# Optimization experiments

Measured on AMD Instinct MI355X. Metric: run time of the kernel, lower is better.

Reference implementation:

```python
import jax, jax.numpy as jnp
import numpy as np


def setup_inputs() -> dict:
    key = jax.random.key(0)
    ks = jax.random.split(key, 8)
    B = 32768
    return {
        "x": jax.random.normal(ks[0], (B, 784), dtype=jnp.float32),
        "conv_w": jax.random.normal(ks[1], (3, 3), dtype=jnp.float32),
        "fc1_w": jax.random.normal(ks[2], (512, 676), dtype=jnp.float32) * 0.04,
        "fc1_b": jax.random.normal(ks[3], (512,), dtype=jnp.float32),
        "fc2_w": jax.random.normal(ks[4], (512, 512), dtype=jnp.float32) * 0.04,
        "fc2_b": jax.random.normal(ks[5], (512,), dtype=jnp.float32),
        "out_w": jax.random.normal(ks[6], (10, 512), dtype=jnp.float32) * 0.04,
        "out_b": jax.random.normal(ks[7], (10,), dtype=jnp.float32),
    }


def reference(x, conv_w, fc1_w, fc1_b, fc2_w, fc2_b, out_w, out_b):
    B = x.shape[0]
    img = x.reshape(B, 1, 28, 28)  # NCHW, single channel
    # Valid 3x3 cross-correlation (same math as the nested tensordot loop).
    kern = conv_w.reshape(1, 1, 3, 3)  # OIHW
    conv = jax.lax.conv_general_dilated(
        img, kern, window_strides=(1, 1), padding="VALID",
        dimension_numbers=("NCHW", "OIHW", "NCHW"))  # [B,1,26,26]
    h = conv.reshape(B, 26 * 26)
    h = jax.nn.relu(h @ fc1_w.T + fc1_b)
    h = jax.nn.relu(h @ fc2_w.T + fc2_b)
    return h @ out_w.T + out_b  # [B,10] logits
```

## Files before the change

kernel.cpp:

```cpp
#include <hip/hip_runtime.h>

typedef unsigned short ushort_t;
typedef __attribute__((ext_vector_type(8))) short bf16x8;
typedef __attribute__((ext_vector_type(4))) float f32x4;
typedef __attribute__((ext_vector_type(16))) float f32x16;

__device__ __forceinline__ unsigned short f2bf(float f) {
    union { float f; unsigned u; } v; v.f = f;
    unsigned r = v.u + 0x7FFFu + ((v.u >> 16) & 1u);
    return (unsigned short)(r >> 16);
}

__global__ __launch_bounds__(256) void prep_w(const float* __restrict__ fc1_w,
                                              const float* __restrict__ cw,
                                              const float* __restrict__ fc2_w,
                                              const float* __restrict__ out_w,
                                              ushort_t* __restrict__ W1,
                                              ushort_t* __restrict__ W2,
                                              ushort_t* __restrict__ W3) {
    const int idx = blockIdx.x * 256 + threadIdx.x;
    if (idx < 512 * 832) {
        int n = idx / 832, p = idx % 832;
        float acc = 0.f;
        if (p < 784) {
            int pr = p / 28, pc = p % 28;
#pragma unroll
            for (int dr = 0; dr < 3; ++dr) {
                int r = pr - dr;
                if (r < 0 || r >= 26) continue;
#pragma unroll
                for (int dc = 0; dc < 3; ++dc) {
                    int col = pc - dc;
                    if (col < 0 || col >= 26) continue;
                    acc += cw[dr * 3 + dc] * fc1_w[n * 676 + r * 26 + col];
                }
            }
        }
        W1[idx] = f2bf(acc);
    }
    if (idx < 512 * 512) W2[idx] = f2bf(fc2_w[idx]);
    if (idx < 16 * 512)  W3[idx] = (idx < 10 * 512) ? f2bf(out_w[idx]) : (ushort_t)0;
}

__global__ __launch_bounds__(512, 2) void mega2(const float* __restrict__ x,
                                                const ushort_t* __restrict__ W1,
                                                const ushort_t* __restrict__ W2,
                                                const ushort_t* __restrict__ W3,
                                                const float* __restrict__ b1,
                                                const float* __restrict__ b2,
                                                const float* __restrict__ ob,
                                                float* __restrict__ out) {
    extern __shared__ ushort_t smem[];
    ushort_t* xs = smem;
    ushort_t* hs = smem + 8192;

    const int tid = threadIdx.x;
    const int wave = tid >> 6, lane = tid & 63;
    const int r32 = lane & 31, khalf = lane >> 5;
    const int xrow = tid >> 3, xoct = tid & 7;
    const int m0 = blockIdx.x * 128;

    f32x16 acc[2][2][2];
#pragma unroll
    for (int a = 0; a < 2; ++a)
#pragma unroll
        for (int i = 0; i < 2; ++i)
#pragma unroll
            for (int j = 0; j < 2; ++j)
#pragma unroll
                for (int e = 0; e < 16; ++e) acc[a][i][j][e] = 0.f;

    f32x4 xv0[2], xv1[2];
    auto load_x = [&](int ks) {
        const int gc = ks * 64 + xoct * 8;
#pragma unroll
        for (int mh = 0; mh < 2; ++mh) {
            if (gc < 784) {
                const f32x4* p = (const f32x4*)&x[(size_t)(m0 + mh * 64 + xrow) * 784 + gc];
                xv0[mh] = __builtin_nontemporal_load(p);
                xv1[mh] = __builtin_nontemporal_load(p + 1);
            } else {
                xv0[mh] = (f32x4){0.f, 0.f, 0.f, 0.f};
                xv1[mh] = (f32x4){0.f, 0.f, 0.f, 0.f};
            }
        }
    };
    load_x(0);

    for (int ks = 0; ks < 13; ++ks) {
#pragma unroll
        for (int mh = 0; mh < 2; ++mh) {
            bf16x8 xv;
            xv[0] = (short)f2bf(xv0[mh].x); xv[1] = (short)f2bf(xv0[mh].y);
            xv[2] = (short)f2bf(xv0[mh].z); xv[3] = (short)f2bf(xv0[mh].w);
            xv[4] = (short)f2bf(xv1[mh].x); xv[5] = (short)f2bf(xv1[mh].y);
            xv[6] = (short)f2bf(xv1[mh].z); xv[7] = (short)f2bf(xv1[mh].w);
            *(bf16x8*)&xs[mh * 4096 + xrow * 64 + ((xoct ^ (xrow & 7)) * 8)] = xv;
        }
        __syncthreads();
        if (ks < 12) load_x(ks + 1);
        const int k0 = ks * 64;
#pragma unroll
        for (int ksub = 0; ksub < 4; ++ksub) {
            const int q = 2 * ksub + khalf;
            bf16x8 bw[2], af[2][2];
#pragma unroll
            for (int j = 0; j < 2; ++j)
                bw[j] = *(const bf16x8*)&W1[(size_t)(wave * 64 + j * 32 + r32) * 832 + k0 + q * 8];
#pragma unroll
            for (int mh = 0; mh < 2; ++mh)
#pragma unroll
                for (int i = 0; i < 2; ++i) {
                    const int mr = i * 32 + r32;
                    af[mh][i] = *(const bf16x8*)&xs[mh * 4096 + mr * 64 + ((q ^ (mr & 7)) * 8)];
                }
#pragma unroll
            for (int mh = 0; mh < 2; ++mh)
#pragma unroll
                for (int i = 0; i < 2; ++i)
#pragma unroll
                    for (int j = 0; j < 2; ++j)
                        acc[mh][i][j] = __builtin_amdgcn_mfma_f32_32x32x16_bf16(af[mh][i], bw[j], acc[mh][i][j], 0, 0, 0);
        }
        __syncthreads();
    }

#pragma unroll
    for (int j = 0; j < 2; ++j) {
        const int n = wave * 64 + j * 32 + r32;
        const float bb = b1[n];
        const int nseg = n >> 3, nrem = n & 7;
#pragma unroll
        for (int mh = 0; mh < 2; ++mh)
#pragma unroll
            for (int i = 0; i < 2; ++i)
#pragma unroll
                for (int reg = 0; reg < 16; ++reg) {
                    const int m = mh * 64 + i * 32 + 4 * khalf + (reg & 3) + 8 * (reg >> 2);
                    hs[m * 512 + ((nseg ^ (m & 7)) * 8) + nrem] = f2bf(fmaxf(acc[mh][i][j][reg] + bb, 0.f));
                }
    }
#pragma unroll
    for (int a = 0; a < 2; ++a)
#pragma unroll
        for (int i = 0; i < 2; ++i)
#pragma unroll
            for (int j = 0; j < 2; ++j)
#pragma unroll
                for (int e = 0; e < 16; ++e) acc[a][i][j][e] = 0.f;
    __syncthreads();

    for (int ks = 0; ks < 8; ++ks) {
        const int k0 = ks * 64;
#pragma unroll
        for (int ksub = 0; ksub < 4; ++ksub) {
            const int q = 2 * ksub + khalf;
            const int hq = ks * 8 + q;
            bf16x8 bw[2], af[2][2];
#pragma unroll
            for (int j = 0; j < 2; ++j)
                bw[j] = *(const bf16x8*)&W2[(size_t)(wave * 64 + j * 32 + r32) * 512 + k0 + q * 8];
#pragma unroll
            for (int mh = 0; mh < 2; ++mh)
#pragma unroll
                for (int i = 0; i < 2; ++i) {
                    const int m = mh * 64 + i * 32 + r32;
                    af[mh][i] = *(const bf16x8*)&hs[m * 512 + ((hq ^ (m & 7)) * 8)];
                }
#pragma unroll
            for (int mh = 0; mh < 2; ++mh)
#pragma unroll
                for (int i = 0; i < 2; ++i)
#pragma unroll
                    for (int j = 0; j < 2; ++j)
                        acc[mh][i][j] = __builtin_amdgcn_mfma_f32_32x32x16_bf16(af[mh][i], bw[j], acc[mh][i][j], 0, 0, 0);
        }
    }
    __syncthreads();

#pragma unroll
    for (int j = 0; j < 2; ++j) {
        const int n = wave * 64 + j * 32 + r32;
        const float bb = b2[n];
        const int nseg = n >> 3, nrem = n & 7;
#pragma unroll
        for (int mh = 0; mh < 2; ++mh)
#pragma unroll
            for (int i = 0; i < 2; ++i)
#pragma unroll
                for (int reg = 0; reg < 16; ++reg) {
                    const int m = mh * 64 + i * 32 + 4 * khalf + (reg & 3) + 8 * (reg >> 2);
                    hs[m * 512 + ((nseg ^ (m & 7)) * 8) + nrem] = f2bf(fmaxf(acc[mh][i][j][reg] + bb, 0.f));
                }
    }
    __syncthreads();

    {
        const int quad = lane >> 4, l16 = lane & 15;
        const int row = wave * 16 + l16;
        f32x4 hacc = {0.f, 0.f, 0.f, 0.f};
#pragma unroll
        for (int ks = 0; ks < 16; ++ks) {
            const int seg = 4 * ks + quad;
            const bf16x8 a = *(const bf16x8*)&hs[row * 512 + ((seg ^ (row & 7)) * 8)];
            const bf16x8 b = *(const bf16x8*)&W3[l16 * 512 + ks * 32 + quad * 8];
            hacc = __builtin_amdgcn_mfma_f32_16x16x32_bf16(a, b, hacc, 0, 0, 0);
        }
        if (l16 < 10) {
            const float bb = ob[l16];
#pragma unroll
            for (int r = 0; r < 4; ++r)
                out[(size_t)(m0 + wave * 16 + quad * 4 + r) * 10 + l16] = hacc[r] + bb;
        }
    }
}

extern "C" void kernel_launch(void* const* d_in, const int* in_sizes, int n_in,
                              void* d_out, int out_size, void* d_ws, size_t ws_size,
                              hipStream_t stream) {
    const float* x      = (const float*)d_in[0];
    const float* conv_w = (const float*)d_in[1];
    const float* fc1_w  = (const float*)d_in[2];
    const float* fc1_b  = (const float*)d_in[3];
    const float* fc2_w  = (const float*)d_in[4];
    const float* fc2_b  = (const float*)d_in[5];
    const float* out_w  = (const float*)d_in[6];
    const float* out_b  = (const float*)d_in[7];
    float* out = (float*)d_out;

    ushort_t* W1 = (ushort_t*)d_ws;
    ushort_t* W2 = W1 + 512 * 832;
    ushort_t* W3 = W2 + 512 * 512;

    prep_w<<<dim3(1664), 256, 0, stream>>>(fc1_w, conv_w, fc2_w, out_w, W1, W2, W3);

    mega2<<<dim3(256), 512, 147456, stream>>>(x, W1, W2, W3, fc1_b, fc2_b, out_b, out);
}
```

Before: 235.7 us.

## Pre-pack weights into MFMA fragment order and double-buffer x tiles

The weight prep kernel writes W1 and W2 in a per-wave fragment layout, so each lane's B-operand load is one contiguous 16-byte read and each wave reads a contiguous 1KB block. The x staging in shared memory is double-buffered, so the next tile is converted and stored while the current one is consumed, leaving one barrier per k-step instead of two. This costs extra shared memory, and the second x buffer reuses the region later used for the hidden activations.

```diff
diff --git a/kernel.cpp b/kernel.cpp
--- a/kernel.cpp
+++ b/kernel.cpp
@@ -36,13 +36,22 @@
                 }
             }
         }
-        W1[idx] = f2bf(acc);
-    }
-    if (idx < 512 * 512) W2[idx] = f2bf(fc2_w[idx]);
+        const int ngrp = n >> 5, r = n & 31;
+        const int kfrag = p >> 4, c = p & 15;
+        const int lane = (c >> 3) * 32 + r;
+        W1[((size_t)ngrp * 52 + kfrag) * 512 + lane * 8 + (c & 7)] = f2bf(acc);
+    }
+    if (idx < 512 * 512) {
+        int n = idx >> 9, p = idx & 511;
+        const int ngrp = n >> 5, r = n & 31;
+        const int kfrag = p >> 4, c = p & 15;
+        const int lane = (c >> 3) * 32 + r;
+        W2[((size_t)ngrp * 32 + kfrag) * 512 + lane * 8 + (c & 7)] = f2bf(fc2_w[idx]);
+    }
     if (idx < 16 * 512)  W3[idx] = (idx < 10 * 512) ? f2bf(out_w[idx]) : (ushort_t)0;
 }
 
-__global__ __launch_bounds__(512, 2) void mega2(const float* __restrict__ x,
+__global__ __launch_bounds__(512, 2) void mega3(const float* __restrict__ x,
                                                 const ushort_t* __restrict__ W1,
                                                 const ushort_t* __restrict__ W2,
                                                 const ushort_t* __restrict__ W3,
@@ -85,9 +94,7 @@
             }
         }
     };
-    load_x(0);
-
-    for (int ks = 0; ks < 13; ++ks) {
+    auto store_x = [&](int buf) {
 #pragma unroll
         for (int mh = 0; mh < 2; ++mh) {
             bf16x8 xv;
@@ -95,24 +102,31 @@
             xv[2] = (short)f2bf(xv0[mh].z); xv[3] = (short)f2bf(xv0[mh].w);
             xv[4] = (short)f2bf(xv1[mh].x); xv[5] = (short)f2bf(xv1[mh].y);
             xv[6] = (short)f2bf(xv1[mh].z); xv[7] = (short)f2bf(xv1[mh].w);
-            *(bf16x8*)&xs[mh * 4096 + xrow * 64 + ((xoct ^ (xrow & 7)) * 8)] = xv;
-        }
-        __syncthreads();
+            *(bf16x8*)&xs[buf * 8192 + mh * 4096 + xrow * 64 + ((xoct ^ (xrow & 7)) * 8)] = xv;
+        }
+    };
+
+    load_x(0);
+    store_x(0);
+    __syncthreads();
+
+    for (int ks = 0; ks < 13; ++ks) {
         if (ks < 12) load_x(ks + 1);
-        const int k0 = ks * 64;
+        const int buf = ks & 1;
 #pragma unroll
         for (int ksub = 0; ksub < 4; ++ksub) {
+            const int kfrag = ks * 4 + ksub;
+            bf16x8 bw[2], af[2][2];
+#pragma unroll
+            for (int j = 0; j < 2; ++j)
+                bw[j] = *(const bf16x8*)&W1[((size_t)(wave * 2 + j) * 52 + kfrag) * 512 + lane * 8];
             const int q = 2 * ksub + khalf;
-            bf16x8 bw[2], af[2][2];
-#pragma unroll
-            for (int j = 0; j < 2; ++j)
-                bw[j] = *(const bf16x8*)&W1[(size_t)(wave * 64 + j * 32 + r32) * 832 + k0 + q * 8];
 #pragma unroll
             for (int mh = 0; mh < 2; ++mh)
 #pragma unroll
                 for (int i = 0; i < 2; ++i) {
                     const int mr = i * 32 + r32;
-                    af[mh][i] = *(const bf16x8*)&xs[mh * 4096 + mr * 64 + ((q ^ (mr & 7)) * 8)];
+                    af[mh][i] = *(const bf16x8*)&xs[buf * 8192 + mh * 4096 + mr * 64 + ((q ^ (mr & 7)) * 8)];
                 }
 #pragma unroll
             for (int mh = 0; mh < 2; ++mh)
@@ -122,9 +136,13 @@
                     for (int j = 0; j < 2; ++j)
                         acc[mh][i][j] = __builtin_amdgcn_mfma_f32_32x32x16_bf16(af[mh][i], bw[j], acc[mh][i][j], 0, 0, 0);
         }
-        __syncthreads();
-    }
-
+        if (ks < 12) {
+            store_x(1 - buf);
+            __syncthreads();
+        }
+    }
+
+    __syncthreads();
 #pragma unroll
     for (int j = 0; j < 2; ++j) {
         const int n = wave * 64 + j * 32 + r32;
@@ -151,15 +169,14 @@
     __syncthreads();
 
     for (int ks = 0; ks < 8; ++ks) {
-        const int k0 = ks * 64;
 #pragma unroll
         for (int ksub = 0; ksub < 4; ++ksub) {
-            const int q = 2 * ksub + khalf;
-            const int hq = ks * 8 + q;
+            const int kfrag = ks * 4 + ksub;
             bf16x8 bw[2], af[2][2];
 #pragma unroll
             for (int j = 0; j < 2; ++j)
-                bw[j] = *(const bf16x8*)&W2[(size_t)(wave * 64 + j * 32 + r32) * 512 + k0 + q * 8];
+                bw[j] = *(const bf16x8*)&W2[((size_t)(wave * 2 + j) * 32 + kfrag) * 512 + lane * 8];
+            const int hq = ks * 8 + 2 * ksub + khalf;
 #pragma unroll
             for (int mh = 0; mh < 2; ++mh)
 #pragma unroll
@@ -234,5 +251,5 @@
 
     prep_w<<<dim3(1664), 256, 0, stream>>>(fc1_w, conv_w, fc2_w, out_w, W1, W2, W3);
 
-    mega2<<<dim3(256), 512, 147456, stream>>>(x, W1, W2, W3, fc1_b, fc2_b, out_b, out);
-}
+    mega3<<<dim3(256), 512, 147456, stream>>>(x, W1, W2, W3, fc1_b, fc2_b, out_b, out);
+}
```

After: 217.4 us. 1.08x faster.

## Use 16 waves per block, pre-swizzle weights into MFMA fragment layout, double-buffer x

Applied to the files above, without the earlier changes.

The block grows from 8 to 16 waves (1024 threads), so each wave owns a 32-column slice of N instead of 64 and keeps half as many accumulators. The prep kernel now writes W1 and W2 in per-fragment order, so each lane's B operand is one contiguous 16-byte load and a wave's loads coalesce. The x tile is double-buffered in LDS, reusing the hs region as the second buffer, which drops one barrier per k-step. The aim is more waves to hide latency and cheaper weight loads, at the cost of more weight traffic per block and tighter register limits at 1024 threads.

```diff
diff --git a/kernel.cpp b/kernel.cpp
--- a/kernel.cpp
+++ b/kernel.cpp
@@ -19,18 +19,23 @@
                                               ushort_t* __restrict__ W2,
                                               ushort_t* __restrict__ W3) {
     const int idx = blockIdx.x * 256 + threadIdx.x;
-    if (idx < 512 * 832) {
-        int n = idx / 832, p = idx % 832;
+    if (idx < 425984) {
+        const int ngrp = idx / 26624;
+        const int kfrag = (idx % 26624) >> 9;
+        const int li = idx & 511;
+        const int lane = li >> 3, e = li & 7;
+        const int n = ngrp * 32 + (lane & 31);
+        const int p = kfrag * 16 + (lane >> 5) * 8 + e;
         float acc = 0.f;
         if (p < 784) {
-            int pr = p / 28, pc = p % 28;
+            const int pr = p / 28, pc = p % 28;
 #pragma unroll
             for (int dr = 0; dr < 3; ++dr) {
-                int r = pr - dr;
+                const int r = pr - dr;
                 if (r < 0 || r >= 26) continue;
 #pragma unroll
                 for (int dc = 0; dc < 3; ++dc) {
-                    int col = pc - dc;
+                    const int col = pc - dc;
                     if (col < 0 || col >= 26) continue;
                     acc += cw[dr * 3 + dc] * fc1_w[n * 676 + r * 26 + col];
                 }
@@ -38,21 +43,29 @@
         }
         W1[idx] = f2bf(acc);
     }
-    if (idx < 512 * 512) W2[idx] = f2bf(fc2_w[idx]);
+    if (idx < 262144) {
+        const int ngrp = idx / 16384;
+        const int kfrag = (idx % 16384) >> 9;
+        const int li = idx & 511;
+        const int lane = li >> 3, e = li & 7;
+        const int n = ngrp * 32 + (lane & 31);
+        const int p = kfrag * 16 + (lane >> 5) * 8 + e;
+        W2[idx] = f2bf(fc2_w[n * 512 + p]);
+    }
     if (idx < 16 * 512)  W3[idx] = (idx < 10 * 512) ? f2bf(out_w[idx]) : (ushort_t)0;
 }
 
-__global__ __launch_bounds__(512, 2) void mega2(const float* __restrict__ x,
-                                                const ushort_t* __restrict__ W1,
-                                                const ushort_t* __restrict__ W2,
-                                                const ushort_t* __restrict__ W3,
-                                                const float* __restrict__ b1,
-                                                const float* __restrict__ b2,
-                                                const float* __restrict__ ob,
-                                                float* __restrict__ out) {
+__global__ __launch_bounds__(1024, 4) void mega4(const float* __restrict__ x,
+                                                 const ushort_t* __restrict__ W1,
+                                                 const ushort_t* __restrict__ W2,
+                                                 const ushort_t* __restrict__ W3,
+                                                 const float* __restrict__ b1,
+                                                 const float* __restrict__ b2,
+                                                 const float* __restrict__ ob,
+                                                 float* __restrict__ out) {
     extern __shared__ ushort_t smem[];
-    ushort_t* xs = smem;
-    ushort_t* hs = smem + 8192;
+    ushort_t* xs0 = smem;
+    ushort_t* hs  = smem + 8192;
 
     const int tid = threadIdx.x;
     const int wave = tid >> 6, lane = tid & 63;
@@ -60,74 +73,70 @@
     const int xrow = tid >> 3, xoct = tid & 7;
     const int m0 = blockIdx.x * 128;
 
-    f32x16 acc[2][2][2];
+    f32x16 acc[2][2];
 #pragma unroll
     for (int a = 0; a < 2; ++a)
 #pragma unroll
         for (int i = 0; i < 2; ++i)
 #pragma unroll
-            for (int j = 0; j < 2; ++j)
-#pragma unroll
-                for (int e = 0; e < 16; ++e) acc[a][i][j][e] = 0.f;
-
-    f32x4 xv0[2], xv1[2];
+            for (int e = 0; e < 16; ++e) acc[a][i][e] = 0.f;
+
+    f32x4 xv0, xv1;
     auto load_x = [&](int ks) {
         const int gc = ks * 64 + xoct * 8;
-#pragma unroll
-        for (int mh = 0; mh < 2; ++mh) {
-            if (gc < 784) {
-                const f32x4* p = (const f32x4*)&x[(size_t)(m0 + mh * 64 + xrow) * 784 + gc];
-                xv0[mh] = __builtin_nontemporal_load(p);
-                xv1[mh] = __builtin_nontemporal_load(p + 1);
-            } else {
-                xv0[mh] = (f32x4){0.f, 0.f, 0.f, 0.f};
-                xv1[mh] = (f32x4){0.f, 0.f, 0.f, 0.f};
-            }
+        if (gc < 784) {
+            const f32x4* p = (const f32x4*)&x[(size_t)(m0 + xrow) * 784 + gc];
+            xv0 = __builtin_nontemporal_load(p);
+            xv1 = __builtin_nontemporal_load(p + 1);
+        } else {
+            xv0 = (f32x4){0.f, 0.f, 0.f, 0.f};
+            xv1 = (f32x4){0.f, 0.f, 0.f, 0.f};
         }
     };
+    auto store_x = [&](ushort_t* buf) {
+        bf16x8 xv;
+        xv[0] = (short)f2bf(xv0.x); xv[1] = (short)f2bf(xv0.y);
+        xv[2] = (short)f2bf(xv0.z); xv[3] = (short)f2bf(xv0.w);
+        xv[4] = (short)f2bf(xv1.x); xv[5] = (short)f2bf(xv1.y);
+        xv[6] = (short)f2bf(xv1.z); xv[7] = (short)f2bf(xv1.w);
+        *(bf16x8*)&buf[xrow * 64 + ((xoct ^ (xrow & 7)) * 8)] = xv;
+    };
+
     load_x(0);
+    store_x(xs0);
+    __syncthreads();
 
     for (int ks = 0; ks < 13; ++ks) {
-#pragma unroll
-        for (int mh = 0; mh < 2; ++mh) {
-            bf16x8 xv;
-            xv[0] = (short)f2bf(xv0[mh].x); xv[1] = (short)f2bf(xv0[mh].y);
-            xv[2] = (short)f2bf(xv0[mh].z); xv[3] = (short)f2bf(xv0[mh].w);
-            xv[4] = (short)f2bf(xv1[mh].x); xv[5] = (short)f2bf(xv1[mh].y);
-            xv[6] = (short)f2bf(xv1[mh].z); xv[7] = (short)f2bf(xv1[mh].w);
-            *(bf16x8*)&xs[mh * 4096 + xrow * 64 + ((xoct ^ (xrow & 7)) * 8)] = xv;
-        }
-        __syncthreads();
         if (ks < 12) load_x(ks + 1);
-        const int k0 = ks * 64;
+        const ushort_t* bufp = (ks & 1) ? hs : xs0;
 #pragma unroll
         for (int ksub = 0; ksub < 4; ++ksub) {
+            const int kfrag = ks * 4 + ksub;
+            const bf16x8 bw = *(const bf16x8*)&W1[((size_t)wave * 52 + kfrag) * 512 + lane * 8];
             const int q = 2 * ksub + khalf;
-            bf16x8 bw[2], af[2][2];
-#pragma unroll
-            for (int j = 0; j < 2; ++j)
-                bw[j] = *(const bf16x8*)&W1[(size_t)(wave * 64 + j * 32 + r32) * 832 + k0 + q * 8];
+            bf16x8 af[2][2];
 #pragma unroll
             for (int mh = 0; mh < 2; ++mh)
 #pragma unroll
                 for (int i = 0; i < 2; ++i) {
-                    const int mr = i * 32 + r32;
-                    af[mh][i] = *(const bf16x8*)&xs[mh * 4096 + mr * 64 + ((q ^ (mr & 7)) * 8)];
+                    const int mr = mh * 64 + i * 32 + r32;
+                    af[mh][i] = *(const bf16x8*)&bufp[mr * 64 + ((q ^ (mr & 7)) * 8)];
                 }
 #pragma unroll
             for (int mh = 0; mh < 2; ++mh)
 #pragma unroll
                 for (int i = 0; i < 2; ++i)
-#pragma unroll
-                    for (int j = 0; j < 2; ++j)
-                        acc[mh][i][j] = __builtin_amdgcn_mfma_f32_32x32x16_bf16(af[mh][i], bw[j], acc[mh][i][j], 0, 0, 0);
-        }
-        __syncthreads();
-    }
-
-#pragma unroll
-    for (int j = 0; j < 2; ++j) {
-        const int n = wave * 64 + j * 32 + r32;
+                    acc[mh][i] = __builtin_amdgcn_mfma_f32_32x32x16_bf16(af[mh][i], bw, acc[mh][i], 0, 0, 0);
+        }
+        if (ks < 12) {
+            store_x((ks & 1) ? xs0 : hs);
+            __syncthreads();
+        }
+    }
+    __syncthreads();
+
+    {
+        const int n = wave * 32 + r32;
         const float bb = b1[n];
         const int nseg = n >> 3, nrem = n & 7;
 #pragma unroll
@@ -137,7 +146,7 @@
 #pragma unroll
                 for (int reg = 0; reg < 16; ++reg) {
                     const int m = mh * 64 + i * 32 + 4 * khalf + (reg & 3) + 8 * (reg >> 2);
-                    hs[m * 512 + ((nseg ^ (m & 7)) * 8) + nrem] = f2bf(fmaxf(acc[mh][i][j][reg] + bb, 0.f));
+                    hs[m * 512 + ((nseg ^ (m & 7)) * 8) + nrem] = f2bf(fmaxf(acc[mh][i][reg] + bb, 0.f));
                 }
     }
 #pragma unroll
@@ -145,21 +154,16 @@
 #pragma unroll
         for (int i = 0; i < 2; ++i)
 #pragma unroll
-            for (int j = 0; j < 2; ++j)
-#pragma unroll
-                for (int e = 0; e < 16; ++e) acc[a][i][j][e] = 0.f;
+            for (int e = 0; e < 16; ++e) acc[a][i][e] = 0.f;
     __syncthreads();
 
     for (int ks = 0; ks < 8; ++ks) {
-        const int k0 = ks * 64;
 #pragma unroll
         for (int ksub = 0; ksub < 4; ++ksub) {
-            const int q = 2 * ksub + khalf;
-            const int hq = ks * 8 + q;
-            bf16x8 bw[2], af[2][2];
-#pragma unroll
-            for (int j = 0; j < 2; ++j)
-                bw[j] = *(const bf16x8*)&W2[(size_t)(wave * 64 + j * 32 + r32) * 512 + k0 + q * 8];
+            const int kfrag = ks * 4 + ksub;
+            const bf16x8 bw = *(const bf16x8*)&W2[((size_t)wave * 32 + kfrag) * 512 + lane * 8];
+            const int hq = ks * 8 + 2 * ksub + khalf;
+            bf16x8 af[2][2];
 #pragma unroll
             for (int mh = 0; mh < 2; ++mh)
 #pragma unroll
@@ -171,16 +175,13 @@
             for (int mh = 0; mh < 2; ++mh)
 #pragma unroll
                 for (int i = 0; i < 2; ++i)
-#pragma unroll
-                    for (int j = 0; j < 2; ++j)
-                        acc[mh][i][j] = __builtin_amdgcn_mfma_f32_32x32x16_bf16(af[mh][i], bw[j], acc[mh][i][j], 0, 0, 0);
-        }
-    }
-    __syncthreads();
-
-#pragma unroll
-    for (int j = 0; j < 2; ++j) {
-        const int n = wave * 64 + j * 32 + r32;
+                    acc[mh][i] = __builtin_amdgcn_mfma_f32_32x32x16_bf16(af[mh][i], bw, acc[mh][i], 0, 0, 0);
+        }
+    }
+    __syncthreads();
+
+    {
+        const int n = wave * 32 + r32;
         const float bb = b2[n];
         const int nseg = n >> 3, nrem = n & 7;
 #pragma unroll
@@ -190,12 +191,12 @@
 #pragma unroll
                 for (int reg = 0; reg < 16; ++reg) {
                     const int m = mh * 64 + i * 32 + 4 * khalf + (reg & 3) + 8 * (reg >> 2);
-                    hs[m * 512 + ((nseg ^ (m & 7)) * 8) + nrem] = f2bf(fmaxf(acc[mh][i][j][reg] + bb, 0.f));
-                }
-    }
-    __syncthreads();
-
-    {
+                    hs[m * 512 + ((nseg ^ (m & 7)) * 8) + nrem] = f2bf(fmaxf(acc[mh][i][reg] + bb, 0.f));
+                }
+    }
+    __syncthreads();
+
+    if (wave < 8) {
         const int quad = lane >> 4, l16 = lane & 15;
         const int row = wave * 16 + l16;
         f32x4 hacc = {0.f, 0.f, 0.f, 0.f};
@@ -229,10 +230,10 @@
     float* out = (float*)d_out;
 
     ushort_t* W1 = (ushort_t*)d_ws;
-    ushort_t* W2 = W1 + 512 * 832;
-    ushort_t* W3 = W2 + 512 * 512;
+    ushort_t* W2 = W1 + 425984;
+    ushort_t* W3 = W2 + 262144;
 
     prep_w<<<dim3(1664), 256, 0, stream>>>(fc1_w, conv_w, fc2_w, out_w, W1, W2, W3);
 
-    mega2<<<dim3(256), 512, 147456, stream>>>(x, W1, W2, W3, fc1_b, fc2_b, out_b, out);
-}
+    mega4<<<dim3(256), 1024, 147456, stream>>>(x, W1, W2, W3, fc1_b, fc2_b, out_b, out);
+}
```

After: 216.1 us. 8.3% less time.
